# Kernel optimization log

Measured on AMD Instinct MI355X. Metric: run time of the kernel, lower is better.

The kernel has to match this reference:

```python
import jax, jax.numpy as jnp
import numpy as np

N = 100000   # nodes
E = 300000   # directed edges (avg degree 3, molecular graphs)
G = 4000     # molecules in the batch
IN = 9
HID = 128
HEADS = 4
NEG_SLOPE = 0.2


def setup_inputs() -> dict:
    key = jax.random.key(0)
    ks = jax.random.split(key, 12)
    x = jax.random.normal(ks[0], (N, IN), dtype=jnp.float32)
    edge_index = jax.random.randint(ks[1], (2, E), 0, N, dtype=jnp.int32)
    batch = jnp.sort(jax.random.randint(ks[2], (N,), 0, G, dtype=jnp.int32))
    s = 0.1  # keep activations in a sane range
    W1 = jax.random.normal(ks[3], (IN, HEADS * HID), dtype=jnp.float32) * s
    a_src1 = jax.random.normal(ks[4], (HEADS, HID), dtype=jnp.float32) * s
    a_dst1 = jax.random.normal(ks[5], (HEADS, HID), dtype=jnp.float32) * s
    b1 = jax.random.normal(ks[6], (HEADS * HID,), dtype=jnp.float32) * s
    W2 = jax.random.normal(ks[7], (HEADS * HID, HID), dtype=jnp.float32) * s
    a_src2 = jax.random.normal(ks[8], (1, HID), dtype=jnp.float32) * s
    a_dst2 = jax.random.normal(ks[9], (1, HID), dtype=jnp.float32) * s
    b2 = jax.random.normal(ks[10], (HID,), dtype=jnp.float32) * s
    return {"x": x, "edge_index": edge_index, "batch": batch,
            "W1": W1, "a_src1": a_src1, "a_dst1": a_dst1, "b1": b1,
            "W2": W2, "a_src2": a_src2, "a_dst2": a_dst2, "b2": b2}


def _gat_conv(x, edge_index, W, a_src, a_dst, b, heads, out_ch, concat):
    """PyG GATConv: linear proj, per-edge leaky-relu attention logits,
    segment softmax over destination nodes, scatter-add aggregation.
    add_self_loops=True (PyG default)."""
    n = x.shape[0]
    loops = jnp.arange(n, dtype=edge_index.dtype)
    src = jnp.concatenate([edge_index[0], loops])
    dst = jnp.concatenate([edge_index[1], loops])

    h = (x @ W).reshape(n, heads, out_ch)                  # [N, H, C]
    alpha_s = jnp.einsum('nhc,hc->nh', h, a_src)           # [N, H]
    alpha_d = jnp.einsum('nhc,hc->nh', h, a_dst)           # [N, H]

    logits = jax.nn.leaky_relu(alpha_s[src] + alpha_d[dst], NEG_SLOPE)  # [Etot, H]
    # numerically stable segment softmax over incoming edges of each dst
    m = jax.ops.segment_max(logits, dst, num_segments=n)   # [N, H] (finite: self-loops)
    e = jnp.exp(logits - m[dst])
    z = jax.ops.segment_sum(e, dst, num_segments=n)
    alpha = e / (z[dst] + 1e-16)                           # [Etot, H]

    msg = h[src] * alpha[:, :, None]                       # [Etot, H, C]
    out = jax.ops.segment_sum(msg, dst, num_segments=n)    # [N, H, C]
    if concat:
        out = out.reshape(n, heads * out_ch)
    else:
        out = out.mean(axis=1)
    return out + b


def reference(x, edge_index, batch, W1, a_src1, a_dst1, b1, W2, a_src2, a_dst2, b2):
    h = jax.nn.elu(_gat_conv(x, edge_index, W1, a_src1, a_dst1, b1, HEADS, HID, True))
    h = jax.nn.elu(_gat_conv(h, edge_index, W2, a_src2, a_dst2, b2, 1, HID, True))
    # global mean pool per graph
    sums = jax.ops.segment_sum(h, batch, num_segments=G)   # [G, HID]
    cnt = jax.ops.segment_sum(jnp.ones((h.shape[0],), h.dtype), batch, num_segments=G)
    return sums / jnp.maximum(cnt, 1.0)[:, None]
```

## Files before the change

### kernel.cpp

```cpp
#include <hip/hip_runtime.h>

#define N_NODES 100000
#define N_EDGES 300000
#define N_GRAPHS 4000
#define CAP 32

typedef float f32x4 __attribute__((ext_vector_type(4)));
typedef float f32x16 __attribute__((ext_vector_type(16)));
typedef __bf16 bf16x8 __attribute__((ext_vector_type(8)));
typedef __bf16 bf16x4 __attribute__((ext_vector_type(4)));
typedef __bf16 bf16x2 __attribute__((ext_vector_type(2)));
typedef _Float16 f16x8 __attribute__((ext_vector_type(8)));

static const size_t OFF_XA    = 0;
static const size_t OFF_AD4   = OFF_XA + (size_t)N_NODES * 16;
static const size_t OFF_P2B   = OFF_AD4 + (size_t)N_NODES * 4;
static const size_t OFF_ASAD2 = OFF_P2B + (size_t)N_NODES * 64;
static const size_t OFF_WSB   = OFF_ASAD2 + (size_t)N_NODES * 2;
static const size_t OFF_W1B   = OFF_WSB + 32768;
static const size_t OFF_GST   = OFF_W1B + 4096;
static const size_t OFF_INT   = OFF_GST + 4096;

#define PRE_NODE_END 391
#define PRE_PACKB_END 455
#define PRE_W1B_END 487
#define PRE_GST_END 503
#define PRE_BKT_END 1675

__device__ __forceinline__ float lrelu(float x) { return x < 0.f ? 0.2f * x : x; }
__device__ __forceinline__ float elu(float x)   { return x > 0.f ? x : __expf(x) - 1.f; }

__global__ __launch_bounds__(256) void k_pre(
    const float* __restrict__ x, const float* __restrict__ W1,
    const float* __restrict__ a_src1, const float* __restrict__ a_dst1,
    const float* __restrict__ W2, const int* __restrict__ batch,
    const int* __restrict__ ei,
    float* __restrict__ xa, float* __restrict__ ad4,
    __bf16* __restrict__ wsB, _Float16* __restrict__ w1b,
    int* __restrict__ deg, int* __restrict__ bucket, int* __restrict__ gstart) {
    int b = blockIdx.x, tid = threadIdx.x;
    if (b < PRE_NODE_END) {
        __shared__ float wf[72];
        if (tid < 72) {
            int isd = tid / 36, r = tid % 36, k = r / 4, h = r % 4;
            const float* a = isd ? a_dst1 : a_src1;
            float s = 0.f;
            for (int c = 0; c < 128; c++) s += W1[k * 512 + h * 128 + c] * a[h * 128 + c];
            wf[tid] = s;
        }
        __syncthreads();
        int n = b * 256 + tid;
        if (n >= N_NODES) return;
        float xv[9];
#pragma unroll
        for (int k = 0; k < 9; k++) xv[k] = x[n * 9 + k];
        float as[4], ad[4];
#pragma unroll
        for (int h = 0; h < 4; h++) {
            float s = 0.f, d = 0.f;
#pragma unroll
            for (int k = 0; k < 9; k++) {
                s += xv[k] * wf[k * 4 + h];
                d += xv[k] * wf[36 + k * 4 + h];
            }
            as[h] = s; ad[h] = d;
        }
        f32x4* xp = (f32x4*)(xa + (size_t)n * 16);
        xp[0] = (f32x4){xv[0], xv[1], xv[2], xv[3]};
        xp[1] = (f32x4){xv[4], xv[5], xv[6], xv[7]};
        xp[2] = (f32x4){xv[8], as[0], as[1], as[2]};
        xp[3] = (f32x4){as[3], 0.f, 0.f, 0.f};
        *(f32x4*)(ad4 + (size_t)n * 4) = (f32x4){ad[0], ad[1], ad[2], ad[3]};
    } else if (b < PRE_PACKB_END) {
        int t = (b - PRE_NODE_END) * 256 + tid;
#pragma unroll
        for (int m = 0; m < 4; m++) {
            int idx = t * 4 + m;
            int k = idx >> 7, nn = idx & 127;
            wsB[(size_t)nn * 512 + k] = (__bf16)W2[(size_t)k * 128 + nn];
        }
    } else if (b < PRE_W1B_END) {
        int t = (b - PRE_PACKB_END) * 256 + tid;
        int j = t >> 4, k = t & 15;
        w1b[t] = (k < 9) ? (_Float16)W1[(size_t)k * 512 + j] : (_Float16)0.f;
    } else if (b < PRE_GST_END) {
        int g = (b - PRE_W1B_END) * 256 + tid;
        if (g > N_GRAPHS) return;
        int lo = 0, hi = N_NODES;
        while (lo < hi) { int mid = (lo + hi) >> 1; if (batch[mid] < g) lo = mid + 1; else hi = mid; }
        gstart[g] = lo;
    } else {
        int e = (b - PRE_GST_END) * 256 + tid;
        if (e >= N_EDGES) return;
        int s = ei[e], d = ei[N_EDGES + e];
        int slot = atomicAdd(&deg[d], 1);
        if (slot < CAP) bucket[d * CAP + slot] = s;
    }
}

__global__ __launch_bounds__(512, 6) void k_gemm(
    const float* __restrict__ xa, const float* __restrict__ ad4,
    const int* __restrict__ deg, const int* __restrict__ bucket,
    const _Float16* __restrict__ w1b, const float* __restrict__ b1,
    const __bf16* __restrict__ wsB,
    const float* __restrict__ a_src2, const float* __restrict__ a_dst2,
    __bf16* __restrict__ p2b, float* __restrict__ asad2) {
    __shared__ __bf16 As[64 * 128];
    __shared__ _Float16 AgF[4 * 64 * 24];
    float* red2 = (float*)AgF;
    const int tid = threadIdx.x;
    const int lane = tid & 63;
    const int w = tid >> 6;
    const int i = lane & 15;
    const int q = lane >> 4;
    const int m0 = blockIdx.x * 64;

    {
        const int r = tid >> 3, sub = tid & 7;
        const int hp = sub & 1;
        const int slot = sub >> 1;
        const int n = m0 + r;
        float acc[2][9] = {};
        float z[2] = {};
        const bool valid = (n < N_NODES);
        if (valid) {
            const float2 adv = *(const float2*)(ad4 + (size_t)n * 4 + hp * 2);
            int dg = deg[n];
            if (dg > CAP) dg = CAP;
#define GATHER1(SRC) do {                                                    \
            const f32x4* xp_ = (const f32x4*)(xa + (size_t)(SRC) * 16);      \
            f32x4 v0 = xp_[0], v1 = xp_[1], v2 = xp_[2], v3 = xp_[3];        \
            float as0 = hp ? v2.w : v2.y;                                    \
            float as1 = hp ? v3.x : v2.z;                                    \
            float e0 = __expf(lrelu(as0 + adv.x));                           \
            float e1 = __expf(lrelu(as1 + adv.y));                           \
            z[0] += e0; z[1] += e1;                                          \
            float xs[9] = {v0.x, v0.y, v0.z, v0.w, v1.x, v1.y, v1.z, v1.w, v2.x}; \
            _Pragma("unroll")                                                \
            for (int k = 0; k < 9; k++) {                                    \
                acc[0][k] += e0 * xs[k]; acc[1][k] += e1 * xs[k];            \
            }                                                                \
        } while (0)
            if (slot == 3) GATHER1(n);
            int j = slot;
            int srcn = (j < dg) ? bucket[n * CAP + j] : -1;
            while (srcn >= 0) {
                int src = srcn;
                j += 4;
                srcn = (j < dg) ? bucket[n * CAP + j] : -1;
                GATHER1(src);
            }
#undef GATHER1
        }
#pragma unroll
        for (int off = 2; off <= 4; off <<= 1) {
#pragma unroll
            for (int h = 0; h < 2; h++) {
                z[h] += __shfl_xor(z[h], off);
#pragma unroll
                for (int k = 0; k < 9; k++) acc[h][k] += __shfl_xor(acc[h][k], off);
            }
        }
        if (sub < 2) {
#pragma unroll
            for (int hh = 0; hh < 2; hh++) {
                float inv = valid ? 1.f / z[hh] : 0.f;
                f16x8 p0, p1;
#pragma unroll
                for (int k = 0; k < 8; k++) { p0[k] = (_Float16)(acc[hh][k] * inv); p1[k] = (_Float16)0.f; }
                p1[0] = (_Float16)(acc[hh][8] * inv);
                _Float16* dst = AgF + (size_t)((sub * 2 + hh) * 64 + r) * 24;
                *(f16x8*)dst = p0;
                *(f16x8*)(dst + 8) = p1;
            }
        }
    }
    __syncthreads();

    f32x4 acc[4];
#pragma unroll
    for (int r = 0; r < 4; r++) acc[r] = (f32x4){0.f, 0.f, 0.f, 0.f};

    const __bf16* bcol = wsB + (size_t)(w * 16 + i) * 512 + q * 8;
    const int nt = w & 1, jt = w >> 1;
    const int l31 = lane & 31, qh = lane >> 5;
    const int ilw = lane & 15, hw = (lane >> 4) & 1;

#pragma unroll
    for (int pass = 0; pass < 4; pass++) {
        bf16x8 breg[4];
#pragma unroll
        for (int kc = 0; kc < 4; kc++)
            breg[kc] = *(const bf16x8*)(bcol + pass * 128 + kc * 32);

        {
            f16x8 av = *(const f16x8*)(w1b + ((size_t)(pass * 128 + jt * 32 + l31) * 16 + qh * 8));
            f16x8 bv = *(const f16x8*)&AgF[(size_t)(pass * 64 + nt * 32 + l31) * 24 + qh * 8];
            f32x16 cfr = (f32x16){0.f, 0.f, 0.f, 0.f, 0.f, 0.f, 0.f, 0.f,
                                  0.f, 0.f, 0.f, 0.f, 0.f, 0.f, 0.f, 0.f};
            cfr = __builtin_amdgcn_mfma_f32_32x32x16_f16(av, bv, cfr, 0, 0, 0);
#pragma unroll
            for (int r2 = 0; r2 < 4; r2++) {
                f32x4 b1v = *(const f32x4*)(b1 + pass * 128 + jt * 32 + r2 * 8 + qh * 4);
                bf16x4 pk;
#pragma unroll
                for (int m = 0; m < 4; m++) pk[m] = (__bf16)elu(cfr[r2 * 4 + m] + b1v[m]);
                *(bf16x4*)&As[(size_t)(((nt * 2 + hw) * 4 + jt) * 512 +
                                       (r2 * 16 + ilw) * 8 + qh * 4)] = pk;
            }
        }
        __syncthreads();

#pragma unroll
        for (int kc = 0; kc < 4; kc++) {
#pragma unroll
            for (int rt = 0; rt < 4; rt++) {
                bf16x8 af = *(const bf16x8*)&As[(rt * 4 + kc) * 512 + lane * 8];
                acc[rt] = __builtin_amdgcn_mfma_f32_16x16x32_bf16(af, breg[kc], acc[rt], 0, 0, 0);
            }
        }
        __syncthreads();
    }

    float as2 = a_src2[w * 16 + i];
    float ad2 = a_dst2[w * 16 + i];
#pragma unroll
    for (int rt = 0; rt < 4; rt++) {
#pragma unroll
        for (int qq = 0; qq < 4; qq++) {
            int r2 = rt * 16 + q * 4 + qq;
            float v = acc[rt][qq];
            if (m0 + r2 < N_NODES)
                p2b[(size_t)(m0 + r2) * 128 + w * 16 + i] = (__bf16)v;
            float s = v * as2, d = v * ad2;
#pragma unroll
            for (int off = 1; off < 16; off <<= 1) {
                s += __shfl_xor(s, off);
                d += __shfl_xor(d, off);
            }
            if (i == 0) {
                red2[r2 * 16 + w * 2] = s;
                red2[r2 * 16 + w * 2 + 1] = d;
            }
        }
    }
    __syncthreads();
    if (tid < 128) {
        int r2 = tid >> 1, cc = tid & 1;
        float sum = 0.f;
#pragma unroll
        for (int ww = 0; ww < 8; ww++) sum += red2[r2 * 16 + ww * 2 + cc];
        if (m0 + r2 < N_NODES) asad2[(size_t)(m0 + r2) * 2 + cc] = sum;
    }
}

__global__ __launch_bounds__(256) void k_agg2pool(
    const __bf16* __restrict__ p2b, const float* __restrict__ asad2,
    const int* __restrict__ deg, const int* __restrict__ bucket,
    const float* __restrict__ b2, const int* __restrict__ gstart,
    float* __restrict__ out) {
    __shared__ float red[4 * 128];
    int g = blockIdx.x;
    int tid = threadIdx.x;
    int wv = __builtin_amdgcn_readfirstlane(tid >> 6);
    int lane = tid & 63;
    int s0n = gstart[g], e0n = gstart[g + 1];
    float b2a = b2[2 * lane], b2b = b2[2 * lane + 1];
    float g0 = 0.f, g1 = 0.f;
    for (int n = s0n + wv; n < e0n; n += 8) {
        const bool hb = (n + 4 < e0n);
        const int nb = hb ? n + 4 : n;
        float lsA = asad2[n * 2],  adA = asad2[n * 2 + 1];
        float lsB = asad2[nb * 2], adB = asad2[nb * 2 + 1];
        int dgA = deg[n];  if (dgA > CAP) dgA = CAP;
        int dgB = hb ? deg[nb] : 0; if (dgB > CAP) dgB = CAP;
        bf16x2 vA = ((const bf16x2*)(p2b + (size_t)n  * 128))[lane];
        bf16x2 vB = ((const bf16x2*)(p2b + (size_t)nb * 128))[lane];
        int4 bkA = *(const int4*)(bucket + (size_t)n  * CAP);
        int4 bkB = *(const int4*)(bucket + (size_t)nb * CAP);
        int sA0 = (dgA > 0) ? bkA.x : n;
        int sA1 = (dgA > 1) ? bkA.y : sA0;
        int sA2 = (dgA > 2) ? bkA.z : sA0;
        int sA3 = (dgA > 3) ? bkA.w : sA0;
        int sB0 = (dgB > 0) ? bkB.x : nb;
        int sB1 = (dgB > 1) ? bkB.y : sB0;
        int sB2 = (dgB > 2) ? bkB.z : sB0;
        int sB3 = (dgB > 3) ? bkB.w : sB0;
        float lA0 = asad2[sA0 * 2], lA1 = asad2[sA1 * 2];
        float lA2 = asad2[sA2 * 2], lA3 = asad2[sA3 * 2];
        float lB0 = asad2[sB0 * 2], lB1 = asad2[sB1 * 2];
        float lB2 = asad2[sB2 * 2], lB3 = asad2[sB3 * 2];
        bf16x2 wA0 = ((const bf16x2*)(p2b + (size_t)sA0 * 128))[lane];
        bf16x2 wA1 = ((const bf16x2*)(p2b + (size_t)sA1 * 128))[lane];
        bf16x2 wA2 = ((const bf16x2*)(p2b + (size_t)sA2 * 128))[lane];
        bf16x2 wA3 = ((const bf16x2*)(p2b + (size_t)sA3 * 128))[lane];
        bf16x2 wB0 = ((const bf16x2*)(p2b + (size_t)sB0 * 128))[lane];
        bf16x2 wB1 = ((const bf16x2*)(p2b + (size_t)sB1 * 128))[lane];
        bf16x2 wB2 = ((const bf16x2*)(p2b + (size_t)sB2 * 128))[lane];
        bf16x2 wB3 = ((const bf16x2*)(p2b + (size_t)sB3 * 128))[lane];
        {
            float e = __expf(lrelu(lsA + adA));
            float z = e;
            float a0 = e * (float)vA.x, a1 = e * (float)vA.y;
            float e0 = (dgA > 0) ? __expf(lrelu(lA0 + adA)) : 0.f;
            float e1 = (dgA > 1) ? __expf(lrelu(lA1 + adA)) : 0.f;
            float e2 = (dgA > 2) ? __expf(lrelu(lA2 + adA)) : 0.f;
            float e3 = (dgA > 3) ? __expf(lrelu(lA3 + adA)) : 0.f;
            z += e0 + e1 + e2 + e3;
            a0 += e0 * (float)wA0.x + e1 * (float)wA1.x + e2 * (float)wA2.x + e3 * (float)wA3.x;
            a1 += e0 * (float)wA0.y + e1 * (float)wA1.y + e2 * (float)wA2.y + e3 * (float)wA3.y;
            for (int j = 4; j < dgA; j += 4) {
                int s0 = bucket[n * CAP + j];
                int s1 = bucket[n * CAP + min(j + 1, dgA - 1)];
                int s2 = bucket[n * CAP + min(j + 2, dgA - 1)];
                int s3 = bucket[n * CAP + min(j + 3, dgA - 1)];
                float l0 = asad2[s0 * 2], l1 = asad2[s1 * 2];
                float l2 = asad2[s2 * 2], l3 = asad2[s3 * 2];
                bf16x2 w0 = ((const bf16x2*)(p2b + (size_t)s0 * 128))[lane];
                bf16x2 w1 = ((const bf16x2*)(p2b + (size_t)s1 * 128))[lane];
                bf16x2 w2 = ((const bf16x2*)(p2b + (size_t)s2 * 128))[lane];
                bf16x2 w3 = ((const bf16x2*)(p2b + (size_t)s3 * 128))[lane];
                float f0 = __expf(lrelu(l0 + adA));
                float f1 = (j + 1 < dgA) ? __expf(lrelu(l1 + adA)) : 0.f;
                float f2 = (j + 2 < dgA) ? __expf(lrelu(l2 + adA)) : 0.f;
                float f3 = (j + 3 < dgA) ? __expf(lrelu(l3 + adA)) : 0.f;
                z += f0 + f1 + f2 + f3;
                a0 += f0 * (float)w0.x + f1 * (float)w1.x + f2 * (float)w2.x + f3 * (float)w3.x;
                a1 += f0 * (float)w0.y + f1 * (float)w1.y + f2 * (float)w2.y + f3 * (float)w3.y;
            }
            float inv = 1.f / z;
            g0 += elu(a0 * inv + b2a);
            g1 += elu(a1 * inv + b2b);
        }
        if (hb) {
            float e = __expf(lrelu(lsB + adB));
            float z = e;
            float a0 = e * (float)vB.x, a1 = e * (float)vB.y;
            float e0 = (dgB > 0) ? __expf(lrelu(lB0 + adB)) : 0.f;
            float e1 = (dgB > 1) ? __expf(lrelu(lB1 + adB)) : 0.f;
            float e2 = (dgB > 2) ? __expf(lrelu(lB2 + adB)) : 0.f;
            float e3 = (dgB > 3) ? __expf(lrelu(lB3 + adB)) : 0.f;
            z += e0 + e1 + e2 + e3;
            a0 += e0 * (float)wB0.x + e1 * (float)wB1.x + e2 * (float)wB2.x + e3 * (float)wB3.x;
            a1 += e0 * (float)wB0.y + e1 * (float)wB1.y + e2 * (float)wB2.y + e3 * (float)wB3.y;
            for (int j = 4; j < dgB; j += 4) {
                int s0 = bucket[nb * CAP + j];
                int s1 = bucket[nb * CAP + min(j + 1, dgB - 1)];
                int s2 = bucket[nb * CAP + min(j + 2, dgB - 1)];
                int s3 = bucket[nb * CAP + min(j + 3, dgB - 1)];
                float l0 = asad2[s0 * 2], l1 = asad2[s1 * 2];
                float l2 = asad2[s2 * 2], l3 = asad2[s3 * 2];
                bf16x2 w0 = ((const bf16x2*)(p2b + (size_t)s0 * 128))[lane];
                bf16x2 w1 = ((const bf16x2*)(p2b + (size_t)s1 * 128))[lane];
                bf16x2 w2 = ((const bf16x2*)(p2b + (size_t)s2 * 128))[lane];
                bf16x2 w3 = ((const bf16x2*)(p2b + (size_t)s3 * 128))[lane];
                float f0 = __expf(lrelu(l0 + adB));
                float f1 = (j + 1 < dgB) ? __expf(lrelu(l1 + adB)) : 0.f;
                float f2 = (j + 2 < dgB) ? __expf(lrelu(l2 + adB)) : 0.f;
                float f3 = (j + 3 < dgB) ? __expf(lrelu(l3 + adB)) : 0.f;
                z += f0 + f1 + f2 + f3;
                a0 += f0 * (float)w0.x + f1 * (float)w1.x + f2 * (float)w2.x + f3 * (float)w3.x;
                a1 += f0 * (float)w0.y + f1 * (float)w1.y + f2 * (float)w2.y + f3 * (float)w3.y;
            }
            float inv = 1.f / z;
            g0 += elu(a0 * inv + b2a);
            g1 += elu(a1 * inv + b2b);
        }
    }
    red[wv * 128 + 2 * lane] = g0;
    red[wv * 128 + 2 * lane + 1] = g1;
    __syncthreads();
    if (tid < 128) {
        float sum = red[tid] + red[128 + tid] + red[256 + tid] + red[384 + tid];
        int cnt = e0n - s0n;
        out[(size_t)g * 128 + tid] = sum / (float)(cnt > 0 ? cnt : 1);
    }
}

extern "C" void kernel_launch(void* const* d_in, const int* in_sizes, int n_in,
                              void* d_out, int out_size, void* d_ws, size_t ws_size,
                              hipStream_t stream) {
    const float* x       = (const float*)d_in[0];
    const int*   ei      = (const int*)d_in[1];
    const int*   batch   = (const int*)d_in[2];
    const float* W1      = (const float*)d_in[3];
    const float* a_src1  = (const float*)d_in[4];
    const float* a_dst1  = (const float*)d_in[5];
    const float* b1      = (const float*)d_in[6];
    const float* W2      = (const float*)d_in[7];
    const float* a_src2  = (const float*)d_in[8];
    const float* a_dst2  = (const float*)d_in[9];
    const float* b2      = (const float*)d_in[10];
    float* out = (float*)d_out;

    float* wsf   = (float*)d_ws;
    float* xa    = wsf + OFF_XA;
    float* ad4   = wsf + OFF_AD4;
    __bf16* p2b  = (__bf16*)(wsf + OFF_P2B);
    float* asad2 = wsf + OFF_ASAD2;
    __bf16* wsB  = (__bf16*)(wsf + OFF_WSB);
    _Float16* w1b = (_Float16*)(wsf + OFF_W1B);
    int* gstart  = (int*)(wsf + OFF_GST);
    int* wsi    = (int*)(wsf + OFF_INT);
    int* deg    = wsi;
    int* bucket = wsi + N_NODES;

    hipMemsetAsync(deg, 0, N_NODES * sizeof(int), stream);
    k_pre<<<PRE_BKT_END, 256, 0, stream>>>(x, W1, a_src1, a_dst1, W2, batch, ei,
                                           xa, ad4, wsB, w1b, deg, bucket, gstart);
    k_gemm<<<(N_NODES + 63) / 64, 512, 0, stream>>>(xa, ad4, deg, bucket, w1b, b1,
                                                    wsB, a_src2, a_dst2, p2b, asad2);
    k_agg2pool<<<N_GRAPHS, 256, 0, stream>>>(p2b, asad2, deg, bucket, b2, gstart, out);
}
```

Measured before the change: 188.4 us.

## Remap layer-1 gather to 8 edge slots per node; widen pooling blocks to 512

In the layer-1 gather phase of k_gemm, each of the 8 threads per node now takes one of 8 edge slots and computes all 4 heads, instead of 4 slots times 2 head-pairs. This cuts redundant source-row loads and spreads edges over more lanes. In exchange it uses more registers (4x9 accumulators), so the occupancy hint is lowered from 6 to 4, and the butterfly reduction covers 3 shuffle stages over 4 heads. k_agg2pool now runs with 512 threads (8 waves) per graph, stepping nodes by 16, with an 8-way final reduction in shared memory.

```diff
diff --git a/kernel.cpp b/kernel.cpp
--- a/kernel.cpp
+++ b/kernel.cpp
@@ -98,7 +98,7 @@
     }
 }
 
-__global__ __launch_bounds__(512, 6) void k_gemm(
+__global__ __launch_bounds__(512, 4) void k_gemm(
     const float* __restrict__ xa, const float* __restrict__ ad4,
     const int* __restrict__ deg, const int* __restrict__ bucket,
     const _Float16* __restrict__ w1b, const float* __restrict__ b1,
@@ -117,59 +117,58 @@
 
     {
         const int r = tid >> 3, sub = tid & 7;
-        const int hp = sub & 1;
-        const int slot = sub >> 1;
         const int n = m0 + r;
-        float acc[2][9] = {};
-        float z[2] = {};
+        float acc0[4][9] = {};
+        float z[4] = {};
         const bool valid = (n < N_NODES);
         if (valid) {
-            const float2 adv = *(const float2*)(ad4 + (size_t)n * 4 + hp * 2);
+            const f32x4 adv = *(const f32x4*)(ad4 + (size_t)n * 4);
             int dg = deg[n];
             if (dg > CAP) dg = CAP;
 #define GATHER1(SRC) do {                                                    \
             const f32x4* xp_ = (const f32x4*)(xa + (size_t)(SRC) * 16);      \
             f32x4 v0 = xp_[0], v1 = xp_[1], v2 = xp_[2], v3 = xp_[3];        \
-            float as0 = hp ? v2.w : v2.y;                                    \
-            float as1 = hp ? v3.x : v2.z;                                    \
-            float e0 = __expf(lrelu(as0 + adv.x));                           \
-            float e1 = __expf(lrelu(as1 + adv.y));                           \
-            z[0] += e0; z[1] += e1;                                          \
+            float e0 = __expf(lrelu(v2.y + adv.x));                          \
+            float e1 = __expf(lrelu(v2.z + adv.y));                          \
+            float e2 = __expf(lrelu(v2.w + adv.z));                          \
+            float e3 = __expf(lrelu(v3.x + adv.w));                          \
+            z[0] += e0; z[1] += e1; z[2] += e2; z[3] += e3;                  \
             float xs[9] = {v0.x, v0.y, v0.z, v0.w, v1.x, v1.y, v1.z, v1.w, v2.x}; \
             _Pragma("unroll")                                                \
             for (int k = 0; k < 9; k++) {                                    \
-                acc[0][k] += e0 * xs[k]; acc[1][k] += e1 * xs[k];            \
+                acc0[0][k] += e0 * xs[k]; acc0[1][k] += e1 * xs[k];          \
+                acc0[2][k] += e2 * xs[k]; acc0[3][k] += e3 * xs[k];          \
             }                                                                \
         } while (0)
-            if (slot == 3) GATHER1(n);
-            int j = slot;
+            if (sub == 7) GATHER1(n);
+            int j = sub;
             int srcn = (j < dg) ? bucket[n * CAP + j] : -1;
             while (srcn >= 0) {
                 int src = srcn;
-                j += 4;
+                j += 8;
                 srcn = (j < dg) ? bucket[n * CAP + j] : -1;
                 GATHER1(src);
             }
 #undef GATHER1
         }
 #pragma unroll
-        for (int off = 2; off <= 4; off <<= 1) {
-#pragma unroll
-            for (int h = 0; h < 2; h++) {
+        for (int off = 1; off < 8; off <<= 1) {
+#pragma unroll
+            for (int h = 0; h < 4; h++) {
                 z[h] += __shfl_xor(z[h], off);
 #pragma unroll
-                for (int k = 0; k < 9; k++) acc[h][k] += __shfl_xor(acc[h][k], off);
-            }
-        }
-        if (sub < 2) {
-#pragma unroll
-            for (int hh = 0; hh < 2; hh++) {
-                float inv = valid ? 1.f / z[hh] : 0.f;
+                for (int k = 0; k < 9; k++) acc0[h][k] += __shfl_xor(acc0[h][k], off);
+            }
+        }
+        if (sub == 0) {
+#pragma unroll
+            for (int h = 0; h < 4; h++) {
+                float inv = valid ? 1.f / z[h] : 0.f;
                 f16x8 p0, p1;
 #pragma unroll
-                for (int k = 0; k < 8; k++) { p0[k] = (_Float16)(acc[hh][k] * inv); p1[k] = (_Float16)0.f; }
-                p1[0] = (_Float16)(acc[hh][8] * inv);
-                _Float16* dst = AgF + (size_t)((sub * 2 + hh) * 64 + r) * 24;
+                for (int k = 0; k < 8; k++) { p0[k] = (_Float16)(acc0[h][k] * inv); p1[k] = (_Float16)0.f; }
+                p1[0] = (_Float16)(acc0[h][8] * inv);
+                _Float16* dst = AgF + (size_t)(h * 64 + r) * 24;
                 *(f16x8*)dst = p0;
                 *(f16x8*)(dst + 8) = p1;
             }
@@ -254,12 +253,12 @@
     }
 }
 
-__global__ __launch_bounds__(256) void k_agg2pool(
+__global__ __launch_bounds__(512) void k_agg2pool(
     const __bf16* __restrict__ p2b, const float* __restrict__ asad2,
     const int* __restrict__ deg, const int* __restrict__ bucket,
     const float* __restrict__ b2, const int* __restrict__ gstart,
     float* __restrict__ out) {
-    __shared__ float red[4 * 128];
+    __shared__ float red[8 * 128];
     int g = blockIdx.x;
     int tid = threadIdx.x;
     int wv = __builtin_amdgcn_readfirstlane(tid >> 6);
@@ -267,9 +266,9 @@
     int s0n = gstart[g], e0n = gstart[g + 1];
     float b2a = b2[2 * lane], b2b = b2[2 * lane + 1];
     float g0 = 0.f, g1 = 0.f;
-    for (int n = s0n + wv; n < e0n; n += 8) {
-        const bool hb = (n + 4 < e0n);
-        const int nb = hb ? n + 4 : n;
+    for (int n = s0n + wv; n < e0n; n += 16) {
+        const bool hb = (n + 8 < e0n);
+        const int nb = hb ? n + 8 : n;
         float lsA = asad2[n * 2],  adA = asad2[n * 2 + 1];
         float lsB = asad2[nb * 2], adB = asad2[nb * 2 + 1];
         int dgA = deg[n];  if (dgA > CAP) dgA = CAP;
@@ -371,7 +370,9 @@
     red[wv * 128 + 2 * lane + 1] = g1;
     __syncthreads();
     if (tid < 128) {
-        float sum = red[tid] + red[128 + tid] + red[256 + tid] + red[384 + tid];
+        float sum = 0.f;
+#pragma unroll
+        for (int ww = 0; ww < 8; ww++) sum += red[ww * 128 + tid];
         int cnt = e0n - s0n;
         out[(size_t)g * 128 + tid] = sum / (float)(cnt > 0 ? cnt : 1);
     }
@@ -410,5 +411,5 @@
                                            xa, ad4, wsB, w1b, deg, bucket, gstart);
     k_gemm<<<(N_NODES + 63) / 64, 512, 0, stream>>>(xa, ad4, deg, bucket, w1b, b1,
                                                     wsB, a_src2, a_dst2, p2b, asad2);
-    k_agg2pool<<<N_GRAPHS, 256, 0, stream>>>(p2b, asad2, deg, bucket, b2, gstart, out);
+    k_agg2pool<<<N_GRAPHS, 512, 0, stream>>>(p2b, asad2, deg, bucket, b2, gstart, out);
 }
```

Result: slower. 205.2 us (+8.9%).
